# Performance work log

Measured on AMD Instinct MI355X. Metric: run time of the kernel, lower is better.

## Reference

```python
import jax, jax.numpy as jnp
import numpy as np

N_SRC = 50000
N_DST = 50000
N_EDGE = 800000
D_SRC = 128
D_DST = 128
D_EDGE = D_SRC + 2 + D_DST  # 258


def setup_inputs() -> dict:
    key = jax.random.key(0)
    ks = jax.random.split(key, 7)
    return {
        "src_node_features": jax.random.normal(ks[0], (N_SRC, D_SRC), jnp.float32),
        "edge_src_idx": jax.random.randint(ks[1], (N_EDGE,), 0, N_SRC, dtype=jnp.int32),
        "dst_node_features": jax.random.normal(ks[2], (N_DST, D_DST), jnp.float32),
        "edge_dst_idx": jax.random.randint(ks[3], (N_EDGE,), 0, N_DST, dtype=jnp.int32),
        "edge_dist_rel": jax.random.normal(ks[4], (N_EDGE, 2), jnp.float32),
        # nn.Linear(258, 1, bias=False) weight stored as a [258] vector
        "w_att": jax.random.normal(ks[5], (D_EDGE,), jnp.float32) * 0.05,
        # nn.Linear(258, 128, bias=False) weight stored transposed [258, 128]
        "w_embed": jax.random.normal(ks[6], (D_EDGE, D_DST), jnp.float32) * 0.05,
    }


def reference(src_node_features, edge_src_idx, dst_node_features, edge_dst_idx,
              edge_dist_rel, w_att, w_embed):
    # Gather endpoint features per edge and concat with relative distance: [E, 258]
    x = jnp.concatenate([
        src_node_features[edge_src_idx],
        edge_dist_rel,
        dst_node_features[edge_dst_idx],
    ], axis=-1)

    # Edge attention score: Linear(258->1, no bias) + LeakyReLU(0.2)
    score = x @ w_att                                     # [E]
    score = jnp.where(score >= 0, score, 0.2 * score)

    # scatter_softmax over destination segments (numerically stable)
    seg_max = jax.ops.segment_max(score, edge_dst_idx, num_segments=N_DST)
    seg_max = jnp.where(jnp.isfinite(seg_max), seg_max, 0.0)  # empty segments
    e = jnp.exp(score - seg_max[edge_dst_idx])
    denom = jax.ops.segment_sum(e, edge_dst_idx, num_segments=N_DST)
    attn = e / denom[edge_dst_idx]                        # [E]
    # Dropout is identity in eval mode.

    # Edge embedding and attention-weighted scatter_add: [N_DST, 128]
    emb = x @ w_embed                                     # [E, 128]
    out = jax.ops.segment_sum(attn[:, None] * emb, edge_dst_idx, num_segments=N_DST)
    return jax.nn.relu(out)
```

## Files before the change

kernel.cpp:

```cpp
#include <hip/hip_runtime.h>
#include <hip/hip_bf16.h>

#define D 128
#define NPB 64
#define EPB1 2048
#define BDST 64
#define CAP 2048
#define MAXBINS 1024

typedef __attribute__((ext_vector_type(8))) short short8;
typedef __attribute__((ext_vector_type(4))) float f32x4;

static __device__ __forceinline__ unsigned short f32_to_bf16(float f) {
    unsigned int u = __float_as_uint(f);
    u = (u + 0x7FFFu + ((u >> 16) & 1u)) >> 16;
    return (unsigned short)u;
}
static __device__ __forceinline__ float bf16lo(unsigned int r) {
    return __uint_as_float(r << 16);
}
static __device__ __forceinline__ float bf16hi(unsigned int r) {
    return __uint_as_float(r & 0xFFFF0000u);
}

__global__ void __launch_bounds__(256)
wconv_kernel(const float* __restrict__ w_embed, unsigned short* __restrict__ w_frag)
{
    int t = blockIdx.x * 256 + threadIdx.x;
    if (t >= 4096) return;
    int set  = t >> 11;
    int ks   = (t >> 9) & 3;
    int nt   = (t >> 6) & 7;
    int lane = t & 63;
    int wrow0 = set ? 130 : 0;
    int col   = nt * 16 + (lane & 15);
    int kbase = ks * 32 + (lane >> 4) * 8;
    unsigned short* dst = w_frag + (size_t)t * 8;
#pragma unroll
    for (int j = 0; j < 8; ++j)
        dst[j] = f32_to_bf16(w_embed[(size_t)(wrow0 + kbase + j) * D + col]);
}

__global__ void __launch_bounds__(256)
proj_both_kernel(const float* __restrict__ src_feat, const float* __restrict__ dst_feat,
                 const unsigned short* __restrict__ wfrag_base,
                 const float* __restrict__ w_att,
                 int n_src, int n_dst, int nblk_src,
                 unsigned short* __restrict__ srcp, unsigned short* __restrict__ dstp,
                 float* __restrict__ src_att, float* __restrict__ dst_att)
{
    const bool is_src = (blockIdx.x < nblk_src);
    const float* feats = is_src ? src_feat : dst_feat;
    const unsigned short* wfrag = is_src ? wfrag_base : wfrag_base + 16384;
    const int wrow = is_src ? 0 : 130;
    const int n_nodes = is_src ? n_src : n_dst;
    unsigned short* proj = is_src ? srcp : dstp;
    float* att = is_src ? src_att : dst_att;
    const int blk = is_src ? blockIdx.x : blockIdx.x - nblk_src;

    __shared__ unsigned short s_tile[NPB * D];
    __shared__ float s_red[NPB][4];

    const int tid = threadIdx.x;
    const int node0 = blk * NPB;

#pragma unroll
    for (int it = 0; it < 8; ++it) {
        int idx = it * 256 + tid;
        int row = idx >> 5, c4 = idx & 31;
        int n = node0 + row;
        float4 v = (n < n_nodes)
                 ? *reinterpret_cast<const float4*>(&feats[(size_t)n * D + c4 * 4])
                 : make_float4(0.f, 0.f, 0.f, 0.f);
        unsigned short h[4];
        h[0] = f32_to_bf16(v.x); h[1] = f32_to_bf16(v.y);
        h[2] = f32_to_bf16(v.z); h[3] = f32_to_bf16(v.w);
        int byte = row * 256 + c4 * 8;
        byte ^= (row & 7) << 4;
        *reinterpret_cast<ushort4*>((char*)s_tile + byte) = *reinterpret_cast<ushort4*>(h);
    }
    __syncthreads();

    const int wv = tid >> 6, lane = tid & 63;

    f32x4 acc[8];
#pragma unroll
    for (int i = 0; i < 8; ++i) acc[i] = {0.f, 0.f, 0.f, 0.f};

    const int arow = wv * 16 + (lane & 15);
#pragma unroll
    for (int ks = 0; ks < 4; ++ks) {
        int abyte = arow * 256 + ks * 64 + (lane >> 4) * 16;
        abyte ^= (arow & 7) << 4;
        short8 a = *reinterpret_cast<const short8*>((char*)s_tile + abyte);
#pragma unroll
        for (int nt = 0; nt < 8; ++nt) {
            short8 b = *reinterpret_cast<const short8*>(wfrag + ((size_t)(ks * 8 + nt) * 64 + lane) * 8);
            acc[nt] = __builtin_amdgcn_mfma_f32_16x16x32_bf16(a, b, acc[nt], 0, 0, 0);
        }
    }

#pragma unroll
    for (int nt = 0; nt < 8; ++nt) {
#pragma unroll
        for (int r = 0; r < 4; ++r) {
            int node = node0 + wv * 16 + (lane >> 4) * 4 + r;
            if (node < n_nodes)
                proj[(size_t)node * D + nt * 16 + (lane & 15)] = f32_to_bf16(acc[nt][r]);
        }
    }

    const int na = tid & 63, kq = tid >> 6;
    float p = 0.f;
#pragma unroll
    for (int k = kq * 32; k < kq * 32 + 32; ++k) {
        int byte = (na * 256 + k * 2) ^ ((na & 7) << 4);
        unsigned short h = *reinterpret_cast<const unsigned short*>((char*)s_tile + byte);
        p += __uint_as_float(((unsigned int)h) << 16) * w_att[wrow + k];
    }
    s_red[na][kq] = p;
    __syncthreads();
    if (tid < NPB) {
        int n = node0 + tid;
        if (n < n_nodes)
            att[n] = s_red[tid][0] + s_red[tid][1] + s_red[tid][2] + s_red[tid][3];
    }
}

__global__ void __launch_bounds__(256)
hist1_kernel(const int* __restrict__ edst, int* __restrict__ bb,
             int n_edge, int nblk1, int nb1)
{
    __shared__ int bins[MAXBINS];
    const int tid = threadIdx.x, blk = blockIdx.x;
    for (int i = tid; i < nb1; i += 256) bins[i] = 0;
    __syncthreads();
#pragma unroll
    for (int it = 0; it < EPB1 / 256; ++it) {
        int e = blk * EPB1 + it * 256 + tid;
        if (e < n_edge) atomicAdd(&bins[((unsigned)edst[e]) >> 6], 1);
    }
    __syncthreads();
    for (int i = tid; i < nb1; i += 256) bb[(size_t)i * nblk1 + blk] = bins[i];
}

__global__ void __launch_bounds__(64)
scan_perbin_kernel(int* __restrict__ bb, int* __restrict__ bintot, int nblk1)
{
    const int bin = blockIdx.x, lane = threadIdx.x;
    const size_t base = (size_t)bin * nblk1;
    int carry = 0;
    for (int s = 0; s < nblk1; s += 64) {
        int idx = s + lane;
        int v = (idx < nblk1) ? bb[base + idx] : 0;
        int x = v;
#pragma unroll
        for (int off = 1; off < 64; off <<= 1) {
            int y = __shfl_up(x, off);
            if (lane >= off) x += y;
        }
        if (idx < nblk1) bb[base + idx] = carry + x - v;
        carry += __shfl(x, 63);
    }
    if (lane == 0) bintot[bin] = carry;
}

__global__ void __launch_bounds__(1024)
scan_bins_kernel(const int* __restrict__ bintot, int* __restrict__ binstart,
                 int nb1, int n_edge)
{
    __shared__ int s_w[16];
    const int tid = threadIdx.x;
    const int lane = tid & 63, wid = tid >> 6;
    int v = (tid < nb1) ? bintot[tid] : 0;
    int x = v;
#pragma unroll
    for (int off = 1; off < 64; off <<= 1) {
        int y = __shfl_up(x, off);
        if (lane >= off) x += y;
    }
    if (lane == 63) s_w[wid] = x;
    __syncthreads();
    if (tid < 16) {
        int w = s_w[tid];
#pragma unroll
        for (int off = 1; off < 16; off <<= 1) {
            int y = __shfl_up(w, off);
            if (tid >= off) w += y;
        }
        s_w[tid] = w - s_w[tid];
    }
    __syncthreads();
    if (tid < nb1) binstart[tid] = s_w[wid] + (x - v);
    if (tid == 0) binstart[nb1] = n_edge;
}

__global__ void __launch_bounds__(256)
pass1_kernel(const int* __restrict__ esrc, const int* __restrict__ edst,
             const float* __restrict__ dist,
             const float* __restrict__ src_att, const float* __restrict__ dst_att,
             const float* __restrict__ w_att,
             const int* __restrict__ bb, const int* __restrict__ binstart,
             float4* __restrict__ meta1, int n_edge, int nblk1, int nb1)
{
    __shared__ int cur[MAXBINS];
    const int tid = threadIdx.x, blk = blockIdx.x;
    for (int i = tid; i < nb1; i += 256)
        cur[i] = binstart[i] + bb[(size_t)i * nblk1 + blk];
    __syncthreads();

    const float wa0 = w_att[128], wa1 = w_att[129];
#pragma unroll
    for (int it = 0; it < EPB1 / 256; ++it) {
        int e = blk * EPB1 + it * 256 + tid;
        if (e < n_edge) {
            int s = esrc[e];
            int d = edst[e];
            float2 dd = *reinterpret_cast<const float2*>(&dist[2 * (size_t)e]);
            float sc = src_att[s] + dst_att[d] + dd.x * wa0 + dd.y * wa1;
            sc = (sc >= 0.f) ? sc : 0.2f * sc;
            float ew = __expf(sc);
            int pos = atomicAdd(&cur[((unsigned)d) >> 6], 1);
            meta1[pos] = make_float4(__int_as_float(s | ((d & 63) << 24)), ew, dd.x, dd.y);
        }
    }
}

__global__ void __launch_bounds__(512)
p2agg_kernel(const float4* __restrict__ meta1, const int* __restrict__ binstart,
             const unsigned short* __restrict__ srcp,
             const unsigned short* __restrict__ dstp,
             const float* __restrict__ w_embed,
             float* __restrict__ out, int n_dst)
{
    __shared__ float4 s_meta[CAP];
    __shared__ int s_cnt[BDST];
    __shared__ int s_ofs[BDST + 1];
    __shared__ int s_cur[BDST];

    const int tid = threadIdx.x;
    const int b = blockIdx.x;
    const int bstart = binstart[b], bend = binstart[b + 1];
    const int bsize = bend - bstart;
    const int lane = tid & 63, wv = tid >> 6;
    const int c0 = 2 * lane;

    const float2 wd0 = *reinterpret_cast<const float2*>(&w_embed[128 * D + c0]);
    const float2 wd1 = *reinterpret_cast<const float2*>(&w_embed[129 * D + c0]);

    if (tid < BDST) s_cnt[tid] = 0;
    __syncthreads();

    if (bsize <= CAP) {
        for (int i = tid; i < bsize; i += 512) {
            int bits = __float_as_int(meta1[bstart + i].x);
            atomicAdd(&s_cnt[((unsigned)bits) >> 24], 1);
        }
        __syncthreads();
        if (tid < BDST) {
            int v = s_cnt[tid];
            int x = v;
#pragma unroll
            for (int off = 1; off < 64; off <<= 1) {
                int y = __shfl_up(x, off);
                if (tid >= off) x += y;
            }
            s_ofs[tid] = x - v;
            s_cur[tid] = x - v;
            if (tid == 63) s_ofs[BDST] = x;
        }
        __syncthreads();
        for (int i = tid; i < bsize; i += 512) {
            float4 m = meta1[bstart + i];
            int dlow = ((unsigned)__float_as_int(m.x)) >> 24;
            int pos = atomicAdd(&s_cur[dlow], 1);
            s_meta[pos] = m;
        }
        __syncthreads();

#define EDGE_ACC(m)                                                               \
        {                                                                         \
            int bits_ = __float_as_int((m).x);                                    \
            unsigned int r_ = *reinterpret_cast<const unsigned int*>(             \
                &srcp[(size_t)(bits_ & 0xFFFFFF) * D + c0]);                      \
            acc0 += (m).y * bf16lo(r_);                                           \
            acc1 += (m).y * bf16hi(r_);                                           \
            sw   += (m).y;                                                        \
            swd0 += (m).y * (m).z;                                                \
            swd1 += (m).y * (m).w;                                                \
        }
#pragma unroll
        for (int k = 0; k < 8; ++k) {
            int dloc = k * 8 + wv;
            int gd = b * BDST + dloc;
            if (gd >= n_dst) continue;
            float2* op = reinterpret_cast<float2*>(&out[(size_t)gd * D + c0]);
            int o0 = s_ofs[dloc], o1 = s_ofs[dloc + 1];
            if (o0 == o1) { *op = make_float2(0.f, 0.f); continue; }

            float acc0 = 0.f, acc1 = 0.f, sw = 0.f, swd0 = 0.f, swd1 = 0.f;
            int j = o0;
            for (; j + 8 <= o1; j += 8) {
                float4 m0 = s_meta[j + 0];
                float4 m1 = s_meta[j + 1];
                float4 m2 = s_meta[j + 2];
                float4 m3 = s_meta[j + 3];
                float4 m4 = s_meta[j + 4];
                float4 m5 = s_meta[j + 5];
                float4 m6 = s_meta[j + 6];
                float4 m7 = s_meta[j + 7];
                EDGE_ACC(m0) EDGE_ACC(m1) EDGE_ACC(m2) EDGE_ACC(m3)
                EDGE_ACC(m4) EDGE_ACC(m5) EDGE_ACC(m6) EDGE_ACC(m7)
            }
            for (; j < o1; ++j) {
                float4 m0 = s_meta[j];
                EDGE_ACC(m0)
            }
            float inv = 1.f / sw;
            unsigned int rd = *reinterpret_cast<const unsigned int*>(&dstp[(size_t)gd * D + c0]);
            float ov0 = (acc0 + swd0 * wd0.x + swd1 * wd1.x) * inv + bf16lo(rd);
            float ov1 = (acc1 + swd0 * wd0.y + swd1 * wd1.y) * inv + bf16hi(rd);
            *op = make_float2(fmaxf(ov0, 0.f), fmaxf(ov1, 0.f));
        }
#undef EDGE_ACC
    } else {
        float acc0[8], acc1[8], sw[8], s0[8], s1[8];
        for (int k = 0; k < 8; ++k) { acc0[k] = acc1[k] = sw[k] = s0[k] = s1[k] = 0.f; }
        for (int cs = bstart; cs < bend; cs += CAP) {
            int n = min(CAP, bend - cs);
            __syncthreads();
            for (int i = tid; i < n; i += 512) s_meta[i] = meta1[cs + i];
            __syncthreads();
            for (int k = 0; k < 8; ++k) {
                int dloc = k * 8 + wv;
                for (int i = 0; i < n; ++i) {
                    float4 m = s_meta[i];
                    int bits = __float_as_int(m.x);
                    if ((int)(((unsigned)bits) >> 24) == dloc) {
                        unsigned int r = *reinterpret_cast<const unsigned int*>(
                            &srcp[(size_t)(bits & 0xFFFFFF) * D + c0]);
                        acc0[k] += m.y * bf16lo(r);
                        acc1[k] += m.y * bf16hi(r);
                        sw[k] += m.y;
                        s0[k] += m.y * m.z;
                        s1[k] += m.y * m.w;
                    }
                }
            }
        }
        for (int k = 0; k < 8; ++k) {
            int dloc = k * 8 + wv;
            int gd = b * BDST + dloc;
            if (gd >= n_dst) continue;
            float2* op = reinterpret_cast<float2*>(&out[(size_t)gd * D + c0]);
            if (sw[k] == 0.f) { *op = make_float2(0.f, 0.f); continue; }
            float inv = 1.f / sw[k];
            unsigned int rd = *reinterpret_cast<const unsigned int*>(&dstp[(size_t)gd * D + c0]);
            float ov0 = (acc0[k] + s0[k] * wd0.x + s1[k] * wd1.x) * inv + bf16lo(rd);
            float ov1 = (acc1[k] + s0[k] * wd0.y + s1[k] * wd1.y) * inv + bf16hi(rd);
            *op = make_float2(fmaxf(ov0, 0.f), fmaxf(ov1, 0.f));
        }
    }
}

extern "C" void kernel_launch(void* const* d_in, const int* in_sizes, int n_in,
                              void* d_out, int out_size, void* d_ws, size_t ws_size,
                              hipStream_t stream)
{
    const float* src_feat = (const float*)d_in[0];
    const int*   esrc     = (const int*)d_in[1];
    const float* dst_feat = (const float*)d_in[2];
    const int*   edst     = (const int*)d_in[3];
    const float* dist     = (const float*)d_in[4];
    const float* w_att    = (const float*)d_in[5];
    const float* w_embed  = (const float*)d_in[6];

    const int n_src  = in_sizes[0] / D;
    const int n_edge = in_sizes[1];
    const int n_dst  = in_sizes[2] / D;

    const int nb1   = (n_dst + BDST - 1) / BDST;
    const int nblk1 = (n_edge + EPB1 - 1) / EPB1;
    const size_t n1 = (size_t)nb1 * nblk1;

    char* p = (char*)d_ws;
    auto carve = [&p](size_t bytes) {
        char* r = p;
        p += (bytes + 255) & ~size_t(255);
        return r;
    };
    unsigned short* src_projb = (unsigned short*)carve((size_t)n_src * D * 2);
    unsigned short* dst_projb = (unsigned short*)carve((size_t)n_dst * D * 2);
    float* src_att   = (float*)carve((size_t)n_src * 4);
    float* dst_att   = (float*)carve((size_t)n_dst * 4);
    int*   bb        = (int*)carve(n1 * 4);
    int*   bintot    = (int*)carve((size_t)nb1 * 4);
    int*   binstart  = (int*)carve((size_t)(nb1 + 1) * 4);
    unsigned short* w_frag = (unsigned short*)carve(2 * 4 * 8 * 64 * 8 * 2);
    float4* meta1    = (float4*)carve((size_t)n_edge * 16);
    (void)ws_size;

    wconv_kernel<<<16, 256, 0, stream>>>(w_embed, w_frag);

    const int nblk_src = (n_src + NPB - 1) / NPB;
    const int nblk_dst = (n_dst + NPB - 1) / NPB;
    proj_both_kernel<<<nblk_src + nblk_dst, 256, 0, stream>>>(
        src_feat, dst_feat, w_frag, w_att, n_src, n_dst, nblk_src,
        src_projb, dst_projb, src_att, dst_att);

    hist1_kernel<<<nblk1, 256, 0, stream>>>(edst, bb, n_edge, nblk1, nb1);

    scan_perbin_kernel<<<nb1, 64, 0, stream>>>(bb, bintot, nblk1);
    scan_bins_kernel<<<1, 1024, 0, stream>>>(bintot, binstart, nb1, n_edge);

    pass1_kernel<<<nblk1, 256, 0, stream>>>(esrc, edst, dist, src_att, dst_att,
                                            w_att, bb, binstart, meta1,
                                            n_edge, nblk1, nb1);

    p2agg_kernel<<<nb1, 512, 0, stream>>>(meta1, binstart, src_projb, dst_projb,
                                          w_embed, (float*)d_out, n_dst);
}
```

Measured before the change: 117.3 us.

## Halve destination bin size and transpose per-block histogram layout for scan

Destination bins shrink from 64 to 32 nodes, doubling the bin count (about 1563) so the aggregation kernel runs twice as many 256-thread blocks instead of 782 blocks of 512 threads. The per-block histogram is stored block-major, and the per-bin scan becomes one thread per bin walking blocks serially with coalesced access. The bin-start scan now loops in chunks of 1024 to handle more bins. The aim is better load balance and occupancy in aggregation and a cheaper histogram scan, at the cost of a longer serial carry loop per thread and more bins to scan.

```diff
diff --git a/kernel.cpp b/kernel.cpp
--- a/kernel.cpp
+++ b/kernel.cpp
@@ -4,9 +4,9 @@
 #define D 128
 #define NPB 64
 #define EPB1 2048
-#define BDST 64
-#define CAP 2048
-#define MAXBINS 1024
+#define BDST 32
+#define CAP 1024
+#define MAXBINS 2048
 
 typedef __attribute__((ext_vector_type(8))) short short8;
 typedef __attribute__((ext_vector_type(4))) float f32x4;
@@ -138,60 +138,68 @@
 #pragma unroll
     for (int it = 0; it < EPB1 / 256; ++it) {
         int e = blk * EPB1 + it * 256 + tid;
-        if (e < n_edge) atomicAdd(&bins[((unsigned)edst[e]) >> 6], 1);
-    }
-    __syncthreads();
-    for (int i = tid; i < nb1; i += 256) bb[(size_t)i * nblk1 + blk] = bins[i];
-}
-
-__global__ void __launch_bounds__(64)
-scan_perbin_kernel(int* __restrict__ bb, int* __restrict__ bintot, int nblk1)
-{
-    const int bin = blockIdx.x, lane = threadIdx.x;
-    const size_t base = (size_t)bin * nblk1;
+        if (e < n_edge) atomicAdd(&bins[((unsigned)edst[e]) >> 5], 1);
+    }
+    __syncthreads();
+    for (int i = tid; i < nb1; i += 256) bb[(size_t)blk * nb1 + i] = bins[i];
+}
+
+__global__ void __launch_bounds__(256)
+carryscan_kernel(int* __restrict__ bb, int* __restrict__ bintot, int nb1, int nblk1)
+{
+    int bin = blockIdx.x * 256 + threadIdx.x;
+    if (bin >= nb1) return;
     int carry = 0;
-    for (int s = 0; s < nblk1; s += 64) {
-        int idx = s + lane;
-        int v = (idx < nblk1) ? bb[base + idx] : 0;
+#pragma unroll 4
+    for (int blk = 0; blk < nblk1; ++blk) {
+        size_t idx = (size_t)blk * nb1 + bin;
+        int v = bb[idx];
+        bb[idx] = carry;
+        carry += v;
+    }
+    bintot[bin] = carry;
+}
+
+__global__ void __launch_bounds__(1024)
+binscan_kernel(const int* __restrict__ bintot, int* __restrict__ binstart,
+               int nb1, int n_edge)
+{
+    __shared__ int s_w[16];
+    __shared__ int s_total;
+    __shared__ int s_carry;
+    const int tid = threadIdx.x;
+    const int lane = tid & 63, wid = tid >> 6;
+    if (tid == 0) s_carry = 0;
+    __syncthreads();
+
+    for (int base = 0; base < nb1; base += 1024) {
+        int idx = base + tid;
+        int v = (idx < nb1) ? bintot[idx] : 0;
         int x = v;
 #pragma unroll
         for (int off = 1; off < 64; off <<= 1) {
             int y = __shfl_up(x, off);
             if (lane >= off) x += y;
         }
-        if (idx < nblk1) bb[base + idx] = carry + x - v;
-        carry += __shfl(x, 63);
-    }
-    if (lane == 0) bintot[bin] = carry;
-}
-
-__global__ void __launch_bounds__(1024)
-scan_bins_kernel(const int* __restrict__ bintot, int* __restrict__ binstart,
-                 int nb1, int n_edge)
-{
-    __shared__ int s_w[16];
-    const int tid = threadIdx.x;
-    const int lane = tid & 63, wid = tid >> 6;
-    int v = (tid < nb1) ? bintot[tid] : 0;
-    int x = v;
-#pragma unroll
-    for (int off = 1; off < 64; off <<= 1) {
-        int y = __shfl_up(x, off);
-        if (lane >= off) x += y;
-    }
-    if (lane == 63) s_w[wid] = x;
-    __syncthreads();
-    if (tid < 16) {
-        int w = s_w[tid];
-#pragma unroll
-        for (int off = 1; off < 16; off <<= 1) {
-            int y = __shfl_up(w, off);
-            if (tid >= off) w += y;
-        }
-        s_w[tid] = w - s_w[tid];
-    }
-    __syncthreads();
-    if (tid < nb1) binstart[tid] = s_w[wid] + (x - v);
+        if (lane == 63) s_w[wid] = x;
+        __syncthreads();
+        if (tid < 16) {
+            int w = s_w[tid];
+            int xi = w;
+#pragma unroll
+            for (int off = 1; off < 16; off <<= 1) {
+                int y = __shfl_up(xi, off);
+                if (tid >= off) xi += y;
+            }
+            if (tid == 15) s_total = xi;
+            s_w[tid] = xi - w;
+        }
+        __syncthreads();
+        if (idx < nb1) binstart[idx] = s_carry + s_w[wid] + (x - v);
+        __syncthreads();
+        if (tid == 0) s_carry += s_total;
+        __syncthreads();
+    }
     if (tid == 0) binstart[nb1] = n_edge;
 }
 
@@ -206,7 +214,7 @@
     __shared__ int cur[MAXBINS];
     const int tid = threadIdx.x, blk = blockIdx.x;
     for (int i = tid; i < nb1; i += 256)
-        cur[i] = binstart[i] + bb[(size_t)i * nblk1 + blk];
+        cur[i] = binstart[i] + bb[(size_t)blk * nb1 + i];
     __syncthreads();
 
     const float wa0 = w_att[128], wa1 = w_att[129];
@@ -220,13 +228,13 @@
             float sc = src_att[s] + dst_att[d] + dd.x * wa0 + dd.y * wa1;
             sc = (sc >= 0.f) ? sc : 0.2f * sc;
             float ew = __expf(sc);
-            int pos = atomicAdd(&cur[((unsigned)d) >> 6], 1);
-            meta1[pos] = make_float4(__int_as_float(s | ((d & 63) << 24)), ew, dd.x, dd.y);
-        }
-    }
-}
-
-__global__ void __launch_bounds__(512)
+            int pos = atomicAdd(&cur[((unsigned)d) >> 5], 1);
+            meta1[pos] = make_float4(__int_as_float(s | ((d & 31) << 24)), ew, dd.x, dd.y);
+        }
+    }
+}
+
+__global__ void __launch_bounds__(256)
 p2agg_kernel(const float4* __restrict__ meta1, const int* __restrict__ binstart,
              const unsigned short* __restrict__ srcp,
              const unsigned short* __restrict__ dstp,
@@ -252,7 +260,7 @@
     __syncthreads();
 
     if (bsize <= CAP) {
-        for (int i = tid; i < bsize; i += 512) {
+        for (int i = tid; i < bsize; i += 256) {
             int bits = __float_as_int(meta1[bstart + i].x);
             atomicAdd(&s_cnt[((unsigned)bits) >> 24], 1);
         }
@@ -261,16 +269,16 @@
             int v = s_cnt[tid];
             int x = v;
 #pragma unroll
-            for (int off = 1; off < 64; off <<= 1) {
+            for (int off = 1; off < BDST; off <<= 1) {
                 int y = __shfl_up(x, off);
                 if (tid >= off) x += y;
             }
             s_ofs[tid] = x - v;
             s_cur[tid] = x - v;
-            if (tid == 63) s_ofs[BDST] = x;
-        }
-        __syncthreads();
-        for (int i = tid; i < bsize; i += 512) {
+            if (tid == BDST - 1) s_ofs[BDST] = x;
+        }
+        __syncthreads();
+        for (int i = tid; i < bsize; i += 256) {
             float4 m = meta1[bstart + i];
             int dlow = ((unsigned)__float_as_int(m.x)) >> 24;
             int pos = atomicAdd(&s_cur[dlow], 1);
@@ -291,7 +299,7 @@
         }
 #pragma unroll
         for (int k = 0; k < 8; ++k) {
-            int dloc = k * 8 + wv;
+            int dloc = k * 4 + wv;
             int gd = b * BDST + dloc;
             if (gd >= n_dst) continue;
             float2* op = reinterpret_cast<float2*>(&out[(size_t)gd * D + c0]);
@@ -329,10 +337,10 @@
         for (int cs = bstart; cs < bend; cs += CAP) {
             int n = min(CAP, bend - cs);
             __syncthreads();
-            for (int i = tid; i < n; i += 512) s_meta[i] = meta1[cs + i];
+            for (int i = tid; i < n; i += 256) s_meta[i] = meta1[cs + i];
             __syncthreads();
             for (int k = 0; k < 8; ++k) {
-                int dloc = k * 8 + wv;
+                int dloc = k * 4 + wv;
                 for (int i = 0; i < n; ++i) {
                     float4 m = s_meta[i];
                     int bits = __float_as_int(m.x);
@@ -349,7 +357,7 @@
             }
         }
         for (int k = 0; k < 8; ++k) {
-            int dloc = k * 8 + wv;
+            int dloc = k * 4 + wv;
             int gd = b * BDST + dloc;
             if (gd >= n_dst) continue;
             float2* op = reinterpret_cast<float2*>(&out[(size_t)gd * D + c0]);
@@ -410,13 +418,13 @@
 
     hist1_kernel<<<nblk1, 256, 0, stream>>>(edst, bb, n_edge, nblk1, nb1);
 
-    scan_perbin_kernel<<<nb1, 64, 0, stream>>>(bb, bintot, nblk1);
-    scan_bins_kernel<<<1, 1024, 0, stream>>>(bintot, binstart, nb1, n_edge);
+    carryscan_kernel<<<(nb1 + 255) / 256, 256, 0, stream>>>(bb, bintot, nb1, nblk1);
+    binscan_kernel<<<1, 1024, 0, stream>>>(bintot, binstart, nb1, n_edge);
 
     pass1_kernel<<<nblk1, 256, 0, stream>>>(esrc, edst, dist, src_att, dst_att,
                                             w_att, bb, binstart, meta1,
                                             n_edge, nblk1, nb1);
 
-    p2agg_kernel<<<nb1, 512, 0, stream>>>(meta1, binstart, src_projb, dst_projb,
+    p2agg_kernel<<<nb1, 256, 0, stream>>>(meta1, binstart, src_projb, dst_projb,
                                           w_embed, (float*)d_out, n_dst);
 }
```

After: 152.2 us. 1.3x slower.
